# Kernel optimization log

Measured on AMD Instinct MI355X. Metric: run time of the kernel, lower is better.

## Reference

```python
import jax, jax.numpy as jnp
import numpy as np

NEG_SLOPE = 0.2  # GAT LeakyReLU slope
EPS = 1e-16


def _pagat_conv(x, path_index, W, a, b, heads, out_ch, concat):
    """Path-augmented GAT conv: attention over (head, mid, tail) path triples,
    messages flow tail -> head, softmax-normalized per destination node."""
    N = x.shape[0]
    head, mid, tail = path_index[0], path_index[1], path_index[2]
    h = (x @ W).reshape(N, heads, out_ch)            # [N, H, C]
    # attention logits from all three path positions: [P, H]
    e = (jnp.einsum('phc,hc->ph', h[head], a[0])
         + jnp.einsum('phc,hc->ph', h[mid], a[1])
         + jnp.einsum('phc,hc->ph', h[tail], a[2]))
    e = jax.nn.leaky_relu(e, NEG_SLOPE)
    # segment softmax over paths grouped by destination (head) node
    m = jax.ops.segment_max(e, head, num_segments=N)  # [N, H]
    ex = jnp.exp(e - m[head])
    s = jax.ops.segment_sum(ex, head, num_segments=N)  # [N, H]
    alpha = ex / (s[head] + EPS)                       # [P, H]
    # aggregate tail features weighted by attention
    out = jax.ops.segment_sum(alpha[..., None] * h[tail], head, num_segments=N)  # [N, H, C]
    if concat:
        out = out.reshape(N, heads * out_ch)
    else:
        out = out.mean(axis=1)
    return out + b


def setup_inputs() -> dict:
    key = jax.random.key(0)
    ks = jax.random.split(key, 8)
    N, F_in, H, C, CLS, P = 100000, 500, 8, 16, 16, 1000000
    x = jax.random.normal(ks[0], (N, F_in), dtype=jnp.float32)
    path_index = jax.random.randint(ks[1], (3, P), 0, N, dtype=jnp.int32)
    W1 = jax.random.normal(ks[2], (F_in, H * C), dtype=jnp.float32) * 0.05
    a1 = jax.random.normal(ks[3], (3, H, C), dtype=jnp.float32) * 0.05
    b1 = jnp.zeros((H * C,), dtype=jnp.float32)
    W2 = jax.random.normal(ks[4], (H * C, CLS), dtype=jnp.float32) * 0.05
    a2 = jax.random.normal(ks[5], (3, 1, CLS), dtype=jnp.float32) * 0.05
    b2 = jnp.zeros((CLS,), dtype=jnp.float32)
    return {"x": x, "path_index": path_index, "W1": W1, "a1": a1, "b1": b1,
            "W2": W2, "a2": a2, "b2": b2}


def reference(x, path_index, W1, a1, b1, W2, a2, b2):
    # eval mode: dropout is identity
    h = _pagat_conv(x, path_index, W1, a1, b1, heads=8, out_ch=16, concat=True)
    h = jax.nn.elu(h)
    h = _pagat_conv(h, path_index, W2, a2, b2, heads=1, out_ch=16, concat=False)
    return jax.nn.log_softmax(h, axis=1)
```

## Files before the change

kernel.cpp:

```cpp
#include <hip/hip_runtime.h>
#include <hip/hip_bf16.h>

#define F_IN  500
#define HC    128
#define NHEAD 8
#define CDIM  16
#define NCLS  16
#define KPAD  512

static __device__ __forceinline__ float bf(const __hip_bfloat16 v) {
    return __bfloat162float(v);
}

static __device__ __forceinline__ unsigned int enc_f32(float f) {
    unsigned int u = __float_as_uint(f);
    return (u & 0x80000000u) ? ~u : (u | 0x80000000u);
}
static __device__ __forceinline__ float dec_f32(unsigned int u) {
    return __uint_as_float((u & 0x80000000u) ? (u & 0x7FFFFFFFu) : ~u);
}

typedef __bf16 bf16x8 __attribute__((ext_vector_type(8)));
typedef float f32x4 __attribute__((ext_vector_type(4)));

static __device__ __forceinline__ void gload16(const void* g, void* l) {
    __builtin_amdgcn_global_load_lds(
        (const __attribute__((address_space(1))) void*)g,
        (__attribute__((address_space(3))) void*)l, 16, 0, 0);
}

__global__ void prep_kernel(const float* __restrict__ W1,
                            __bf16* __restrict__ w1t_hi,
                            __bf16* __restrict__ w1t_lo,
                            int* __restrict__ zp, int nz)
{
    int id = blockIdx.x * 256 + threadIdx.x;
    if (id < HC * KPAD) {
        int c = id >> 9, k = id & 511;
        float v = (k < F_IN) ? W1[k * HC + c] : 0.f;
        __bf16 h = (__bf16)v;
        w1t_hi[id] = h;
        w1t_lo[id] = (__bf16)(v - (float)h);
    }
    if (id < nz) zp[id] = 0;
}

static __device__ __forceinline__ void split8(const float4 a, const float4 b,
                                              bf16x8& hi, bf16x8& lo) {
    float v[8] = {a.x, a.y, a.z, a.w, b.x, b.y, b.z, b.w};
#pragma unroll
    for (int j = 0; j < 8; j++) {
        __bf16 h = (__bf16)v[j];
        hi[j] = h;
        lo[j] = (__bf16)(v[j] - (float)h);
    }
}

__global__ __launch_bounds__(256, 2) void gemm1_v3(
    const float* __restrict__ x,
    const __bf16* __restrict__ w1hi, const __bf16* __restrict__ w1lo,
    const float* __restrict__ zpad,
    __hip_bfloat16* __restrict__ h1, int N)
{
    __shared__ float As[3][64 * 32];
    __shared__ __bf16 BsH[3][128 * 32];
    __shared__ __bf16 BsL[3][128 * 32];

    const int tid = threadIdx.x;
    const int lane = tid & 63, wave = tid >> 6;
    const int m = lane & 15, q = lane >> 4;
    const int wr = wave >> 1, wc = wave & 1;
    const int n0 = blockIdx.x * 64;
    const int woff = wave << 10;

    auto stage = [&](int buf, int t) {
        const int k0 = t * 32;
#pragma unroll
        for (int j = 0; j < 2; ++j) {
            int idx = j * 256 + tid;
            {
                int r = idx >> 3, ps = idx & 7;
                int ls = ps ^ (r & 7);
                int kk = k0 + ls * 4;
                int grow = n0 + r;
                const float* src = (kk < F_IN)
                    ? (x + (size_t)(grow < N ? grow : 0) * F_IN + kk)
                    : zpad;
                gload16(src, (char*)&As[buf][0] + j * 4096 + woff);
            }
            {
                int c = idx >> 2, ps2 = idx & 3;
                int ls2 = ps2 ^ (c & 3);
                gload16(w1hi + c * KPAD + k0 + ls2 * 8, (char*)&BsH[buf][0] + j * 4096 + woff);
                gload16(w1lo + c * KPAD + k0 + ls2 * 8, (char*)&BsL[buf][0] + j * 4096 + woff);
            }
        }
    };

    f32x4 acc[2][4];
#pragma unroll
    for (int rt = 0; rt < 2; ++rt)
#pragma unroll
        for (int ct = 0; ct < 4; ++ct) acc[rt][ct] = (f32x4){0.f, 0.f, 0.f, 0.f};

    stage(0, 0);
    stage(1, 1);

#pragma unroll
    for (int t = 0; t < 16; ++t) {
        if (t > 0) __builtin_amdgcn_s_barrier();
        if (t + 2 < 16) stage((t + 2) % 3, t + 2);
        if (t < 14)       asm volatile("s_waitcnt vmcnt(12)" ::: "memory");
        else if (t == 14) asm volatile("s_waitcnt vmcnt(6)" ::: "memory");
        else              asm volatile("s_waitcnt vmcnt(0)" ::: "memory");
        __builtin_amdgcn_s_barrier();

        const int cur = t % 3;
        bf16x8 ah[2], al[2];
#pragma unroll
        for (int rt = 0; rt < 2; ++rt) {
            int r = wr * 32 + rt * 16 + m;
            int x7 = r & 7;
            const float4* rowp = (const float4*)&As[cur][r * 32];
            float4 f0 = rowp[(2 * q) ^ x7];
            float4 f1 = rowp[(2 * q + 1) ^ x7];
            split8(f0, f1, ah[rt], al[rt]);
        }
        bf16x8 bh[4], bl[4];
#pragma unroll
        for (int ct = 0; ct < 4; ++ct) {
            int c = wc * 64 + ct * 16 + m;
            int s = q ^ (c & 3);
            bh[ct] = *(const bf16x8*)&BsH[cur][c * 32 + s * 8];
            bl[ct] = *(const bf16x8*)&BsL[cur][c * 32 + s * 8];
        }
        __builtin_amdgcn_s_setprio(1);
#pragma unroll
        for (int rt = 0; rt < 2; ++rt)
#pragma unroll
            for (int ct = 0; ct < 4; ++ct) {
                acc[rt][ct] = __builtin_amdgcn_mfma_f32_16x16x32_bf16(ah[rt], bh[ct], acc[rt][ct], 0, 0, 0);
                acc[rt][ct] = __builtin_amdgcn_mfma_f32_16x16x32_bf16(ah[rt], bl[ct], acc[rt][ct], 0, 0, 0);
                acc[rt][ct] = __builtin_amdgcn_mfma_f32_16x16x32_bf16(al[rt], bh[ct], acc[rt][ct], 0, 0, 0);
            }
        __builtin_amdgcn_s_setprio(0);
    }

#pragma unroll
    for (int rt = 0; rt < 2; ++rt) {
        int rbase = n0 + wr * 32 + rt * 16 + q * 4;
#pragma unroll
        for (int ct = 0; ct < 4; ++ct) {
            int col = wc * 64 + ct * 16 + m;
#pragma unroll
            for (int r = 0; r < 4; ++r) {
                int row = rbase + r;
                if (row < N)
                    h1[(size_t)row * HC + col] = __float2bfloat16(acc[rt][ct][r]);
            }
        }
    }
}

__global__ void dots1_kernel(const __hip_bfloat16* __restrict__ h1,
                             const float* __restrict__ a1,
                             float* __restrict__ d1,
                             unsigned int* __restrict__ gmax, int N)
{
    __shared__ unsigned int sm[16];
    if (threadIdx.x < 16) sm[threadIdx.x] = 0;
    __syncthreads();
    int id = blockIdx.x * blockDim.x + threadIdx.x;
    if (id < N * NHEAD) {
        int n = id >> 3, h = id & 7;
        const __hip_bfloat16* hp = h1 + (size_t)n * HC + h * CDIM;
        float s0 = 0.f, s1 = 0.f, s2 = 0.f;
#pragma unroll
        for (int c = 0; c < CDIM; c++) {
            float v = bf(hp[c]);
            s0 += v * a1[(0 * NHEAD + h) * CDIM + c];
            s1 += v * a1[(1 * NHEAD + h) * CDIM + c];
            s2 += v * a1[(2 * NHEAD + h) * CDIM + c];
        }
        d1[id] = s0;
        d1[N * NHEAD + id] = s1;
        d1[2 * N * NHEAD + id] = s2;
        atomicMax(&sm[h], enc_f32(s1));
        atomicMax(&sm[8 + h], enc_f32(s2));
    }
    __syncthreads();
    if (threadIdx.x < 16) atomicMax(&gmax[threadIdx.x], sm[threadIdx.x]);
}

__global__ void hist_kernel(const int* __restrict__ pidx, int* __restrict__ deg, int P) {
    int p = blockIdx.x * blockDim.x + threadIdx.x;
    if (p < P) atomicAdd(deg + pidx[p], 1);
}

__global__ void scan1_kernel(const int* __restrict__ deg, int* __restrict__ start,
                             int* __restrict__ bsum, int N) {
    __shared__ int sh[256];
    int i = blockIdx.x * 256 + threadIdx.x;
    int v = (i < N) ? deg[i] : 0;
    sh[threadIdx.x] = v;
    __syncthreads();
#pragma unroll
    for (int off = 1; off < 256; off <<= 1) {
        int x = (threadIdx.x >= off) ? sh[threadIdx.x - off] : 0;
        __syncthreads();
        sh[threadIdx.x] += x;
        __syncthreads();
    }
    if (i < N) start[i] = sh[threadIdx.x] - v;
    if (threadIdx.x == 255) bsum[blockIdx.x] = sh[255];
}

__global__ void scan2_kernel(int* __restrict__ bsum, int nb) {
    __shared__ int sh[512];
    int v = (threadIdx.x < nb) ? bsum[threadIdx.x] : 0;
    sh[threadIdx.x] = v;
    __syncthreads();
#pragma unroll
    for (int off = 1; off < 512; off <<= 1) {
        int x = (threadIdx.x >= off) ? sh[threadIdx.x - off] : 0;
        __syncthreads();
        sh[threadIdx.x] += x;
        __syncthreads();
    }
    if (threadIdx.x < nb) bsum[threadIdx.x] = sh[threadIdx.x] - v;
}

__global__ void scan3_kernel(int* __restrict__ start, const int* __restrict__ bsum, int N) {
    int i = blockIdx.x * 256 + threadIdx.x;
    if (i < N) start[i] += bsum[blockIdx.x];
}

__global__ void scatter_kernel(const int* __restrict__ pidx,
                               const int* __restrict__ start,
                               int* __restrict__ cursor,
                               int* __restrict__ csr, int P) {
    int p = blockIdx.x * blockDim.x + threadIdx.x;
    if (p >= P) return;
    int hd = pidx[p];
    int pos = atomicAdd(cursor + hd, 1);
    csr[start[hd] + pos] = p;
}

__global__ __launch_bounds__(256) void attn1_csr_kernel(
    const int* __restrict__ csr, const int* __restrict__ start,
    const int* __restrict__ deg, const int* __restrict__ pidx,
    const float* __restrict__ d1, const __hip_bfloat16* __restrict__ h1,
    const float* __restrict__ b1, const unsigned int* __restrict__ gmax,
    float* __restrict__ elu_out, int N, int P)
{
    int node = blockIdx.x * 4 + (threadIdx.x >> 6);
    if (node >= N) return;
    int lane = threadIdx.x & 63;
    int h = lane >> 3;
    int s0 = start[node], dg = deg[node];
    const float* d1m = d1 + (size_t)N * NHEAD;
    const float* d1t = d1 + (size_t)2 * N * NHEAD;
    const float dh = d1[node * NHEAD + h];
    float zub = dh + dec_f32(gmax[h]) + dec_f32(gmax[8 + h]);
    const float mxub = zub > 0.f ? zub : 0.2f * zub;

    float acc0 = 0.f, acc1 = 0.f, den = 0.f;
    for (int k0 = 0; k0 < dg; k0 += 8) {
        int kk = k0 + (lane & 7);
        bool valid = kk < dg;
        int p = csr[s0 + (valid ? kk : dg - 1)];
        int mid = pidx[P + p], tl = pidx[2 * P + p];
        float z = dh + d1m[mid * NHEAD + h] + d1t[tl * NHEAD + h];
        float e = z > 0.f ? z : 0.2f * z;
        float ex = valid ? __expf(e - mxub) : 0.f;
        den += ex;
#pragma unroll
        for (int dk = 0; dk < 8; dk++) {
            int tl_b = __shfl(tl, dk, 8);
            float ex_b = __shfl(ex, dk, 8);
            __hip_bfloat162 v = *(const __hip_bfloat162*)(h1 + (size_t)tl_b * HC + 2 * lane);
            acc0 += ex_b * bf(v.x);
            acc1 += ex_b * bf(v.y);
        }
    }
#pragma unroll
    for (int w = 1; w < 8; w <<= 1) den += __shfl_xor(den, w, 8);

    float inv = 1.f / (den + 1e-16f);
    int j0 = 2 * lane;
    float v0 = acc0 * inv + b1[j0];
    float v1 = acc1 * inv + b1[j0 + 1];
    v0 = v0 > 0.f ? v0 : __expf(v0) - 1.f;
    v1 = v1 > 0.f ? v1 : __expf(v1) - 1.f;
    *(float2*)(elu_out + (size_t)node * HC + j0) = make_float2(v0, v1);
}

__global__ __launch_bounds__(256) void layer2_kernel(
    const float* __restrict__ elu, const float* __restrict__ W2,
    const float* __restrict__ a2,
    float* __restrict__ h2, float* __restrict__ d2,
    unsigned int* __restrict__ gmax2, int N)
{
    __shared__ float rows[16][HC + 1];
    __shared__ float h2s[16][NCLS + 1];
    __shared__ unsigned int smax[2];
    const int n0 = blockIdx.x * 16;
    const int tid = threadIdx.x;
    if (tid < 2) smax[tid] = 0;
    for (int idx = tid; idx < 16 * HC; idx += 256) {
        int r = idx >> 7, c = idx & 127;
        rows[r][c] = (n0 + r < N) ? elu[(size_t)(n0 + r) * HC + c] : 0.f;
    }
    __syncthreads();
    int ln = tid >> 4, c = tid & 15;
    float acc = 0.f;
#pragma unroll 8
    for (int j = 0; j < HC; j++) acc += rows[ln][j] * W2[j * NCLS + c];
    h2s[ln][c] = acc;
    if (n0 + ln < N) h2[(size_t)(n0 + ln) * NCLS + c] = acc;
    __syncthreads();
    if (tid < 48) {
        int l = tid / 3, j = tid - l * 3;
        if (n0 + l < N) {
            float s = 0.f;
#pragma unroll
            for (int cc = 0; cc < NCLS; cc++) s += h2s[l][cc] * a2[j * NCLS + cc];
            d2[j * N + n0 + l] = s;
            if (j) atomicMax(&smax[j - 1], enc_f32(s));
        }
    }
    __syncthreads();
    if (tid < 2) atomicMax(&gmax2[tid], smax[tid]);
}

__global__ __launch_bounds__(256) void attn2_csr_kernel(
    const int* __restrict__ csr, const int* __restrict__ start,
    const int* __restrict__ deg, const int* __restrict__ pidx,
    const float* __restrict__ d2, const float* __restrict__ h2,
    const float* __restrict__ b2, const unsigned int* __restrict__ gmax2,
    float* __restrict__ out, int N, int P)
{
    int node = blockIdx.x * 16 + (threadIdx.x >> 4);
    if (node >= N) return;
    int c = threadIdx.x & 15;
    int s0 = start[node], dg = deg[node];
    const float dh = d2[node];
    const float* d2m = d2 + N;
    const float* d2t = d2 + 2 * N;
    float zub = dh + dec_f32(gmax2[0]) + dec_f32(gmax2[1]);
    const float mxub = zub > 0.f ? zub : 0.2f * zub;

    float acc = 0.f, den = 0.f;
    for (int k0 = 0; k0 < dg; k0 += 16) {
        int kk = k0 + c;
        bool valid = kk < dg;
        int p = csr[s0 + (valid ? kk : dg - 1)];
        int mid = pidx[P + p], tl = pidx[2 * P + p];
        float z = dh + d2m[mid] + d2t[tl];
        float e = z > 0.f ? z : 0.2f * z;
        float ex = valid ? __expf(e - mxub) : 0.f;
        den += ex;
#pragma unroll
        for (int dk = 0; dk < 16; dk++) {
            int tl_b = __shfl(tl, dk, 16);
            float ex_b = __shfl(ex, dk, 16);
            acc += ex_b * h2[(size_t)tl_b * NCLS + c];
        }
    }
#pragma unroll
    for (int w = 1; w < 16; w <<= 1) den += __shfl_xor(den, w, 16);

    float o = acc / (den + 1e-16f) + b2[c];
    float m2 = o;
#pragma unroll
    for (int w = 1; w < 16; w <<= 1) m2 = fmaxf(m2, __shfl_xor(m2, w, 16));
    float ex = __expf(o - m2), sm = ex;
#pragma unroll
    for (int w = 1; w < 16; w <<= 1) sm += __shfl_xor(sm, w, 16);
    float r = o - m2 - __logf(sm);
    out[(size_t)node * NCLS + c] = r;
}

extern "C" void kernel_launch(void* const* d_in, const int* in_sizes, int n_in,
                              void* d_out, int out_size, void* d_ws, size_t ws_size,
                              hipStream_t stream)
{
    const float* x  = (const float*)d_in[0];
    const int*   pi = (const int*)d_in[1];
    const float* W1 = (const float*)d_in[2];
    const float* a1 = (const float*)d_in[3];
    const float* b1 = (const float*)d_in[4];
    const float* W2 = (const float*)d_in[5];
    const float* a2 = (const float*)d_in[6];
    const float* b2 = (const float*)d_in[7];

    const int N = in_sizes[0] / F_IN;
    const int P = in_sizes[1] / 3;

    float* ws = (float*)d_ws;
    size_t off_h1     = 0;
    size_t off_d1     = (size_t)64 * N;
    size_t off_elu    = (size_t)88 * N;
    size_t off_h2     = (size_t)216 * N;
    size_t off_d2     = (size_t)232 * N;
    size_t off_deg    = (size_t)235 * N;
    size_t off_start  = (size_t)236 * N;
    size_t off_cursor = (size_t)237 * N;
    size_t off_gmax   = (size_t)238 * N;
    size_t off_zpad   = (size_t)238 * N + 32;
    size_t off_bsum   = (size_t)238 * N + 96;
    size_t off_csr    = (size_t)238 * N + 96 + 1024;
    size_t off_w1th   = off_csr + P;
    size_t off_w1tl   = off_w1th + 32768;

    __hip_bfloat16* h1 = (__hip_bfloat16*)(ws + off_h1);
    float* d1   = ws + off_d1;
    float* elu  = ws + off_elu;
    float* h2   = ws + off_h2;
    float* d2   = ws + off_d2;
    int* deg    = (int*)(ws + off_deg);
    int* start  = (int*)(ws + off_start);
    int* cursor = (int*)(ws + off_cursor);
    unsigned int* gmax  = (unsigned int*)(ws + off_gmax);
    unsigned int* gmax2 = (unsigned int*)(ws + off_gmax) + 16;
    float* zpad = ws + off_zpad;
    int* bsum   = (int*)(ws + off_bsum);
    int* csr    = (int*)(ws + off_csr);
    __bf16* w1t_hi = (__bf16*)(ws + off_w1th);
    __bf16* w1t_lo = (__bf16*)(ws + off_w1tl);

    const int BLK = 256;
    const int nb = (N + 255) / 256;
    const int nz = 3 * N + 96;

    prep_kernel<<<(nz + 255) / 256, 256, 0, stream>>>(W1, w1t_hi, w1t_lo, deg, nz);
    gemm1_v3<<<(N + 63) / 64, 256, 0, stream>>>(x, w1t_hi, w1t_lo, zpad, h1, N);
    dots1_kernel<<<(N * NHEAD + BLK - 1) / BLK, BLK, 0, stream>>>(h1, a1, d1, gmax, N);
    hist_kernel<<<(P + BLK - 1) / BLK, BLK, 0, stream>>>(pi, deg, P);
    scan1_kernel<<<nb, 256, 0, stream>>>(deg, start, bsum, N);
    scan2_kernel<<<1, 512, 0, stream>>>(bsum, nb);
    scan3_kernel<<<nb, 256, 0, stream>>>(start, bsum, N);
    scatter_kernel<<<(P + BLK - 1) / BLK, BLK, 0, stream>>>(pi, start, cursor, csr, P);
    attn1_csr_kernel<<<(N + 3) / 4, 256, 0, stream>>>(csr, start, deg, pi, d1, h1, b1, gmax, elu, N, P);
    layer2_kernel<<<(N + 15) / 16, 256, 0, stream>>>(elu, W2, a2, h2, d2, gmax2, N);
    attn2_csr_kernel<<<(N + 15) / 16, 256, 0, stream>>>(csr, start, deg, pi, d2, h2, b2, gmax2,
                                                        (float*)d_out, N, P);
}
```

Baseline: 721.0 us.

## Rework GEMM1 pipeline with register-prefetch double buffering and direct B loads

The first-layer GEMM no longer uses triple-buffered direct-to-LDS async loads for both operands. It prefetches the x tile two steps ahead through registers into a double-buffered LDS array, and reads the bf16 hi/lo weight fragments straight from global memory (expected to hit in cache). LDS use falls, so occupancy is raised to 4 blocks per CU. The attention aggregation loops also gain a fully unrolled fast path for full chunks and a trimmed loop for partial chunks, so fewer wasted gathers are issued for padded entries. The risk is that per-iteration global loads of the weight fragments add latency, and the register prefetch exposes load latency that the async LDS path used to hide.

```diff
diff --git a/kernel.cpp b/kernel.cpp
--- a/kernel.cpp
+++ b/kernel.cpp
@@ -22,12 +22,6 @@
 
 typedef __bf16 bf16x8 __attribute__((ext_vector_type(8)));
 typedef float f32x4 __attribute__((ext_vector_type(4)));
-
-static __device__ __forceinline__ void gload16(const void* g, void* l) {
-    __builtin_amdgcn_global_load_lds(
-        (const __attribute__((address_space(1))) void*)g,
-        (__attribute__((address_space(3))) void*)l, 16, 0, 0);
-}
 
 __global__ void prep_kernel(const float* __restrict__ W1,
                             __bf16* __restrict__ w1t_hi,
@@ -56,46 +50,25 @@
     }
 }
 
-__global__ __launch_bounds__(256, 2) void gemm1_v3(
+__global__ __launch_bounds__(256, 4) void gemm1_v4(
     const float* __restrict__ x,
     const __bf16* __restrict__ w1hi, const __bf16* __restrict__ w1lo,
-    const float* __restrict__ zpad,
     __hip_bfloat16* __restrict__ h1, int N)
 {
-    __shared__ float As[3][64 * 32];
-    __shared__ __bf16 BsH[3][128 * 32];
-    __shared__ __bf16 BsL[3][128 * 32];
+    __shared__ float As[2][64 * 32];
 
     const int tid = threadIdx.x;
     const int lane = tid & 63, wave = tid >> 6;
     const int m = lane & 15, q = lane >> 4;
     const int wr = wave >> 1, wc = wave & 1;
     const int n0 = blockIdx.x * 64;
-    const int woff = wave << 10;
-
-    auto stage = [&](int buf, int t) {
-        const int k0 = t * 32;
-#pragma unroll
-        for (int j = 0; j < 2; ++j) {
-            int idx = j * 256 + tid;
-            {
-                int r = idx >> 3, ps = idx & 7;
-                int ls = ps ^ (r & 7);
-                int kk = k0 + ls * 4;
-                int grow = n0 + r;
-                const float* src = (kk < F_IN)
-                    ? (x + (size_t)(grow < N ? grow : 0) * F_IN + kk)
-                    : zpad;
-                gload16(src, (char*)&As[buf][0] + j * 4096 + woff);
-            }
-            {
-                int c = idx >> 2, ps2 = idx & 3;
-                int ls2 = ps2 ^ (c & 3);
-                gload16(w1hi + c * KPAD + k0 + ls2 * 8, (char*)&BsH[buf][0] + j * 4096 + woff);
-                gload16(w1lo + c * KPAD + k0 + ls2 * 8, (char*)&BsL[buf][0] + j * 4096 + woff);
-            }
-        }
-    };
+
+    const int sr = tid >> 2, sp = tid & 3;
+    long arow = n0 + sr; if (arow >= N) arow = 0;
+    const float* aptr = x + arow * F_IN + sp * 8;
+
+    const __bf16* bhb = w1hi + (size_t)(wc * 64 + m) * KPAD + q * 8;
+    const __bf16* blb = w1lo + (size_t)(wc * 64 + m) * KPAD + q * 8;
 
     f32x4 acc[2][4];
 #pragma unroll
@@ -103,19 +76,23 @@
 #pragma unroll
         for (int ct = 0; ct < 4; ++ct) acc[rt][ct] = (f32x4){0.f, 0.f, 0.f, 0.f};
 
-    stage(0, 0);
-    stage(1, 1);
+    float4 nxt0, nxt1;
+    {
+        float4 c0 = *(const float4*)(aptr);
+        float4 c1 = *(const float4*)(aptr + 4);
+        float4* dst = (float4*)&As[0][sr * 32];
+        dst[(2 * sp) ^ (sr & 7)] = c0;
+        dst[(2 * sp + 1) ^ (sr & 7)] = c1;
+        nxt0 = *(const float4*)(aptr + 32);
+        nxt1 = *(const float4*)(aptr + 36);
+        asm volatile("s_waitcnt lgkmcnt(0)" ::: "memory");
+        __builtin_amdgcn_s_barrier();
+    }
 
 #pragma unroll
     for (int t = 0; t < 16; ++t) {
-        if (t > 0) __builtin_amdgcn_s_barrier();
-        if (t + 2 < 16) stage((t + 2) % 3, t + 2);
-        if (t < 14)       asm volatile("s_waitcnt vmcnt(12)" ::: "memory");
-        else if (t == 14) asm volatile("s_waitcnt vmcnt(6)" ::: "memory");
-        else              asm volatile("s_waitcnt vmcnt(0)" ::: "memory");
-        __builtin_amdgcn_s_barrier();
-
-        const int cur = t % 3;
+        const int cur = t & 1;
+
         bf16x8 ah[2], al[2];
 #pragma unroll
         for (int rt = 0; rt < 2; ++rt) {
@@ -129,11 +106,30 @@
         bf16x8 bh[4], bl[4];
 #pragma unroll
         for (int ct = 0; ct < 4; ++ct) {
-            int c = wc * 64 + ct * 16 + m;
-            int s = q ^ (c & 3);
-            bh[ct] = *(const bf16x8*)&BsH[cur][c * 32 + s * 8];
-            bl[ct] = *(const bf16x8*)&BsL[cur][c * 32 + s * 8];
-        }
+            bh[ct] = *(const bf16x8*)(bhb + ct * 16 * KPAD + t * 32);
+            bl[ct] = *(const bf16x8*)(blb + ct * 16 * KPAD + t * 32);
+        }
+        float4 fut0 = make_float4(0.f, 0.f, 0.f, 0.f);
+        float4 fut1 = make_float4(0.f, 0.f, 0.f, 0.f);
+        if (t < 13) {
+            fut0 = *(const float4*)(aptr + (t + 2) * 32);
+            fut1 = *(const float4*)(aptr + (t + 2) * 32 + 4);
+        } else if (t == 13) {
+            float v[8];
+#pragma unroll
+            for (int j = 0; j < 8; j++) {
+                int k = 15 * 32 + sp * 8 + j;
+                v[j] = (k < F_IN) ? aptr[15 * 32 + j] : 0.f;
+            }
+            fut0 = make_float4(v[0], v[1], v[2], v[3]);
+            fut1 = make_float4(v[4], v[5], v[6], v[7]);
+        }
+        if (t < 15) {
+            float4* dst = (float4*)&As[cur ^ 1][sr * 32];
+            dst[(2 * sp) ^ (sr & 7)] = nxt0;
+            dst[(2 * sp + 1) ^ (sr & 7)] = nxt1;
+        }
+
         __builtin_amdgcn_s_setprio(1);
 #pragma unroll
         for (int rt = 0; rt < 2; ++rt)
@@ -144,6 +140,12 @@
                 acc[rt][ct] = __builtin_amdgcn_mfma_f32_16x16x32_bf16(al[rt], bh[ct], acc[rt][ct], 0, 0, 0);
             }
         __builtin_amdgcn_s_setprio(0);
+
+        if (t < 15) {
+            asm volatile("s_waitcnt lgkmcnt(0)" ::: "memory");
+            __builtin_amdgcn_s_barrier();
+        }
+        nxt0 = fut0; nxt1 = fut1;
     }
 
 #pragma unroll
@@ -274,13 +276,24 @@
         float e = z > 0.f ? z : 0.2f * z;
         float ex = valid ? __expf(e - mxub) : 0.f;
         den += ex;
-#pragma unroll
-        for (int dk = 0; dk < 8; dk++) {
-            int tl_b = __shfl(tl, dk, 8);
-            float ex_b = __shfl(ex, dk, 8);
-            __hip_bfloat162 v = *(const __hip_bfloat162*)(h1 + (size_t)tl_b * HC + 2 * lane);
-            acc0 += ex_b * bf(v.x);
-            acc1 += ex_b * bf(v.y);
+        int kmax = dg - k0; if (kmax > 8) kmax = 8;
+        if (kmax == 8) {
+#pragma unroll
+            for (int dk = 0; dk < 8; dk++) {
+                int tl_b = __shfl(tl, dk, 8);
+                float ex_b = __shfl(ex, dk, 8);
+                __hip_bfloat162 v = *(const __hip_bfloat162*)(h1 + (size_t)tl_b * HC + 2 * lane);
+                acc0 += ex_b * bf(v.x);
+                acc1 += ex_b * bf(v.y);
+            }
+        } else {
+            for (int dk = 0; dk < kmax; dk++) {
+                int tl_b = __shfl(tl, dk, 8);
+                float ex_b = __shfl(ex, dk, 8);
+                __hip_bfloat162 v = *(const __hip_bfloat162*)(h1 + (size_t)tl_b * HC + 2 * lane);
+                acc0 += ex_b * bf(v.x);
+                acc1 += ex_b * bf(v.y);
+            }
         }
     }
 #pragma unroll
@@ -360,11 +373,20 @@
         float e = z > 0.f ? z : 0.2f * z;
         float ex = valid ? __expf(e - mxub) : 0.f;
         den += ex;
-#pragma unroll
-        for (int dk = 0; dk < 16; dk++) {
-            int tl_b = __shfl(tl, dk, 16);
-            float ex_b = __shfl(ex, dk, 16);
-            acc += ex_b * h2[(size_t)tl_b * NCLS + c];
+        int kmax = dg - k0; if (kmax > 16) kmax = 16;
+        if (kmax == 16) {
+#pragma unroll
+            for (int dk = 0; dk < 16; dk++) {
+                int tl_b = __shfl(tl, dk, 16);
+                float ex_b = __shfl(ex, dk, 16);
+                acc += ex_b * h2[(size_t)tl_b * NCLS + c];
+            }
+        } else {
+            for (int dk = 0; dk < kmax; dk++) {
+                int tl_b = __shfl(tl, dk, 16);
+                float ex_b = __shfl(ex, dk, 16);
+                acc += ex_b * h2[(size_t)tl_b * NCLS + c];
+            }
         }
     }
 #pragma unroll
@@ -407,7 +429,6 @@
     size_t off_start  = (size_t)236 * N;
     size_t off_cursor = (size_t)237 * N;
     size_t off_gmax   = (size_t)238 * N;
-    size_t off_zpad   = (size_t)238 * N + 32;
     size_t off_bsum   = (size_t)238 * N + 96;
     size_t off_csr    = (size_t)238 * N + 96 + 1024;
     size_t off_w1th   = off_csr + P;
@@ -423,7 +444,6 @@
     int* cursor = (int*)(ws + off_cursor);
     unsigned int* gmax  = (unsigned int*)(ws + off_gmax);
     unsigned int* gmax2 = (unsigned int*)(ws + off_gmax) + 16;
-    float* zpad = ws + off_zpad;
     int* bsum   = (int*)(ws + off_bsum);
     int* csr    = (int*)(ws + off_csr);
     __bf16* w1t_hi = (__bf16*)(ws + off_w1th);
@@ -434,7 +454,7 @@
     const int nz = 3 * N + 96;
 
     prep_kernel<<<(nz + 255) / 256, 256, 0, stream>>>(W1, w1t_hi, w1t_lo, deg, nz);
-    gemm1_v3<<<(N + 63) / 64, 256, 0, stream>>>(x, w1t_hi, w1t_lo, zpad, h1, N);
+    gemm1_v4<<<(N + 63) / 64, 256, 0, stream>>>(x, w1t_hi, w1t_lo, h1, N);
     dots1_kernel<<<(N * NHEAD + BLK - 1) / BLK, BLK, 0, stream>>>(h1, a1, d1, gmax, N);
     hist_kernel<<<(P + BLK - 1) / BLK, BLK, 0, stream>>>(pi, deg, P);
     scan1_kernel<<<nb, 256, 0, stream>>>(deg, start, bsum, N);
```

Result: slower. 772.4 us (+7.1%).

## Batch LDS reads in GEMM with inline asm and trim padded attention gathers

Applied to the files above, without the earlier changes.

The GEMM inner loop now issues all A and B fragment loads as explicit ds_read_b128 instructions with precomputed LDS offsets and waits once before the fp32-to-bf16 split and the MFMAs, so the LDS reads overlap each other. Separately, both attention kernels limit the per-chunk gather loop to the valid path count instead of always running 8 or 16 iterations, which skips useless gathers of padding entries for low-degree nodes. The trade-off is that those loops are no longer unrolled and their trip count varies, and the volatile asm with a full lgkmcnt(0) wait restricts compiler scheduling.

```diff
diff --git a/kernel.cpp b/kernel.cpp
--- a/kernel.cpp
+++ b/kernel.cpp
@@ -27,6 +27,17 @@
     __builtin_amdgcn_global_load_lds(
         (const __attribute__((address_space(1))) void*)g,
         (__attribute__((address_space(3))) void*)l, 16, 0, 0);
+}
+
+static __device__ __forceinline__ unsigned ldsoff(const void* p) {
+    return (unsigned)(size_t)(const __attribute__((address_space(3))) void*)p;
+}
+
+static __device__ __forceinline__ void ds_read_f4(unsigned addr, float4& out) {
+    asm volatile("ds_read_b128 %0, %1" : "=v"(out) : "v"(addr) : "memory");
+}
+static __device__ __forceinline__ void ds_read_bf8(unsigned addr, bf16x8& out) {
+    asm volatile("ds_read_b128 %0, %1" : "=v"(out) : "v"(addr) : "memory");
 }
 
 __global__ void prep_kernel(const float* __restrict__ W1,
@@ -56,7 +67,7 @@
     }
 }
 
-__global__ __launch_bounds__(256, 2) void gemm1_v3(
+__global__ __launch_bounds__(256, 2) void gemm1_v5(
     const float* __restrict__ x,
     const __bf16* __restrict__ w1hi, const __bf16* __restrict__ w1lo,
     const float* __restrict__ zpad,
@@ -97,6 +108,26 @@
         }
     };
 
+    unsigned abase[3], hbase[3], lbase[3];
+#pragma unroll
+    for (int i = 0; i < 3; ++i) {
+        abase[i] = ldsoff(&As[i][0]);
+        hbase[i] = ldsoff(&BsH[i][0]);
+        lbase[i] = ldsoff(&BsL[i][0]);
+    }
+    unsigned aoffs[2][2], boffs[4];
+#pragma unroll
+    for (int rt = 0; rt < 2; ++rt) {
+        int r = wr * 32 + rt * 16 + m, x7 = r & 7;
+        aoffs[rt][0] = r * 128 + (((2 * q) ^ x7) << 4);
+        aoffs[rt][1] = r * 128 + (((2 * q + 1) ^ x7) << 4);
+    }
+#pragma unroll
+    for (int ct = 0; ct < 4; ++ct) {
+        int c = wc * 64 + ct * 16 + m;
+        boffs[ct] = c * 64 + ((q ^ (c & 3)) << 4);
+    }
+
     f32x4 acc[2][4];
 #pragma unroll
     for (int rt = 0; rt < 2; ++rt)
@@ -116,24 +147,24 @@
         __builtin_amdgcn_s_barrier();
 
         const int cur = t % 3;
+        float4 fa[2][2];
+        ds_read_f4(abase[cur] + aoffs[0][0], fa[0][0]);
+        ds_read_f4(abase[cur] + aoffs[0][1], fa[0][1]);
+        ds_read_f4(abase[cur] + aoffs[1][0], fa[1][0]);
+        ds_read_f4(abase[cur] + aoffs[1][1], fa[1][1]);
+        bf16x8 bh[4], bl[4];
+#pragma unroll
+        for (int ct = 0; ct < 4; ++ct) {
+            ds_read_bf8(hbase[cur] + boffs[ct], bh[ct]);
+            ds_read_bf8(lbase[cur] + boffs[ct], bl[ct]);
+        }
+        asm volatile("s_waitcnt lgkmcnt(0)" ::: "memory");
+        __builtin_amdgcn_sched_barrier(0);
+
         bf16x8 ah[2], al[2];
-#pragma unroll
-        for (int rt = 0; rt < 2; ++rt) {
-            int r = wr * 32 + rt * 16 + m;
-            int x7 = r & 7;
-            const float4* rowp = (const float4*)&As[cur][r * 32];
-            float4 f0 = rowp[(2 * q) ^ x7];
-            float4 f1 = rowp[(2 * q + 1) ^ x7];
-            split8(f0, f1, ah[rt], al[rt]);
-        }
-        bf16x8 bh[4], bl[4];
-#pragma unroll
-        for (int ct = 0; ct < 4; ++ct) {
-            int c = wc * 64 + ct * 16 + m;
-            int s = q ^ (c & 3);
-            bh[ct] = *(const bf16x8*)&BsH[cur][c * 32 + s * 8];
-            bl[ct] = *(const bf16x8*)&BsL[cur][c * 32 + s * 8];
-        }
+        split8(fa[0][0], fa[0][1], ah[0], al[0]);
+        split8(fa[1][0], fa[1][1], ah[1], al[1]);
+
         __builtin_amdgcn_s_setprio(1);
 #pragma unroll
         for (int rt = 0; rt < 2; ++rt)
@@ -274,8 +305,8 @@
         float e = z > 0.f ? z : 0.2f * z;
         float ex = valid ? __expf(e - mxub) : 0.f;
         den += ex;
-#pragma unroll
-        for (int dk = 0; dk < 8; dk++) {
+        int kmax = dg - k0; if (kmax > 8) kmax = 8;
+        for (int dk = 0; dk < kmax; dk++) {
             int tl_b = __shfl(tl, dk, 8);
             float ex_b = __shfl(ex, dk, 8);
             __hip_bfloat162 v = *(const __hip_bfloat162*)(h1 + (size_t)tl_b * HC + 2 * lane);
@@ -360,8 +391,8 @@
         float e = z > 0.f ? z : 0.2f * z;
         float ex = valid ? __expf(e - mxub) : 0.f;
         den += ex;
-#pragma unroll
-        for (int dk = 0; dk < 16; dk++) {
+        int kmax = dg - k0; if (kmax > 16) kmax = 16;
+        for (int dk = 0; dk < kmax; dk++) {
             int tl_b = __shfl(tl, dk, 16);
             float ex_b = __shfl(ex, dk, 16);
             acc += ex_b * h2[(size_t)tl_b * NCLS + c];
@@ -434,7 +465,7 @@
     const int nz = 3 * N + 96;
 
     prep_kernel<<<(nz + 255) / 256, 256, 0, stream>>>(W1, w1t_hi, w1t_lo, deg, nz);
-    gemm1_v3<<<(N + 63) / 64, 256, 0, stream>>>(x, w1t_hi, w1t_lo, zpad, h1, N);
+    gemm1_v5<<<(N + 63) / 64, 256, 0, stream>>>(x, w1t_hi, w1t_lo, zpad, h1, N);
     dots1_kernel<<<(N * NHEAD + BLK - 1) / BLK, BLK, 0, stream>>>(h1, a1, d1, gmax, N);
     hist_kernel<<<(P + BLK - 1) / BLK, BLK, 0, stream>>>(pi, deg, P);
     scan1_kernel<<<nb, 256, 0, stream>>>(deg, start, bsum, N);
```

New measurement: 727.9 us. About the same (+1.0%).
